# Kernel tuning notes

Hardware: AMD Instinct MI355X
Metric: run time of the kernel (lower is better)

## Reference

```python
import jax, jax.numpy as jnp
import numpy as np

INV_SQRT2 = 0.7071067811865476


def _dense(x, W):
    return jax.nn.silu(x @ W)


def _residual(x, Wa, Wb):
    # GemNet ResidualLayer: two activated dense layers, skip, 1/sqrt(2) rescale
    return (x + _dense(_dense(x, Wa), Wb)) * INV_SQRT2


def setup_inputs() -> dict:
    key = jax.random.key(0)
    ks = iter(jax.random.split(key, 40))
    N, E, T = 10000, 200000, 400000
    NR, NS = 128, 7          # num_radial, num_spherical
    A, M, Ti, To, C = 128, 256, 64, 64, 16
    NB = 2                   # num_blocks

    def w(shape):
        fan_in = shape[-2]
        return jax.random.normal(next(ks), shape, jnp.float32) / float(np.sqrt(fan_in))

    inp = {}
    inp['atomic_numbers'] = jax.random.randint(next(ks), (N,), 0, 120)
    inp['idx_s'] = jax.random.randint(next(ks), (E,), 0, N)
    inp['idx_t'] = jax.random.randint(next(ks), (E,), 0, N)
    inp['id3_ba'] = jax.random.randint(next(ks), (T,), 0, E)
    inp['id3_ca'] = jax.random.randint(next(ks), (T,), 0, E)
    inp['rbf'] = jax.random.uniform(next(ks), (E, NR), jnp.float32)
    inp['cbf'] = jax.random.normal(next(ks), (T, NS), jnp.float32)
    V = jax.random.normal(next(ks), (E, 3), jnp.float32)
    inp['V_st'] = V / jnp.linalg.norm(V, axis=-1, keepdims=True)
    inp['atom_table'] = jax.random.normal(next(ks), (120, A), jnp.float32)
    inp['W_edge_in'] = w((2 * A + NR, M))
    inp['rbf_w3'] = w((NB, NR, M))
    inp['W_down'] = w((NB, M, Ti))
    inp['W_cbf'] = w((NB, NS, C))
    inp['W_bil'] = jax.random.normal(next(ks), (NB, C, Ti, To), jnp.float32) / float(np.sqrt(C * Ti))
    inp['W_up'] = w((NB, To, M))
    inp['W_res_e'] = w((NB, 4, M, M))
    inp['rbf_wh'] = w((NB, NR, M))
    inp['W_e2a'] = w((NB, M, A))
    inp['W_res_a'] = w((NB, 2, A, A))
    inp['W_outE_in'] = w((A * (NB + 1), A))
    inp['W_outE_res'] = w((2, A, A))
    inp['W_outE_fin'] = w((A, 1))
    inp['W_outF_in'] = w((M * (NB + 1), M))
    inp['W_outF_res'] = w((2, M, M))
    inp['W_outF_fin'] = w((M, 1))
    return inp


def reference(atomic_numbers, idx_s, idx_t, id3_ba, id3_ca, rbf, cbf, V_st,
              atom_table, W_edge_in, rbf_w3, W_down, W_cbf, W_bil, W_up,
              W_res_e, rbf_wh, W_e2a, W_res_a,
              W_outE_in, W_outE_res, W_outE_fin,
              W_outF_in, W_outF_res, W_outF_fin):
    N = atomic_numbers.shape[0]
    E = idx_s.shape[0]
    NB = rbf_w3.shape[0]

    # atom and edge embeddings
    h = atom_table[atomic_numbers]                                       # [N, A]
    m = _dense(jnp.concatenate([h[idx_s], h[idx_t], rbf], axis=-1), W_edge_in)  # [E, M]

    xs_E = [h]
    xs_F = [m]
    for b in range(NB):
        # --- triplet interaction: edge -> triplet gather, bilinear CBF mix, scatter back ---
        x = (m * (rbf @ rbf_w3[b])) @ W_down[b]                          # [E, Ti]
        cb = cbf @ W_cbf[b]                                              # [T, C]
        y = jnp.einsum('tc,ti,cio->to', cb, x[id3_ba], W_bil[b])         # [T, To]
        agg = jax.ops.segment_sum(y, id3_ca, num_segments=E)             # [E, To]
        x3 = _dense(agg @ W_up[b], jnp.eye(x3_dim := W_up[b].shape[1], dtype=m.dtype)) if False else jax.nn.silu(agg @ W_up[b])  # [E, M]
        # --- residual / skip structure ---
        m2 = _residual(m, W_res_e[b, 0], W_res_e[b, 1])
        m2 = (m2 + x3) * INV_SQRT2
        m = _residual(m2, W_res_e[b, 2], W_res_e[b, 3])
        # --- atom update: edge -> atom scatter ---
        xa = (m * (rbf @ rbf_wh[b])) @ W_e2a[b]                          # [E, A]
        ha = jax.ops.segment_sum(xa, idx_t, num_segments=N)              # [N, A]
        h = h + _residual(ha, W_res_a[b, 0], W_res_a[b, 1])
        xs_E.append(h)
        xs_F.append(m)

    # FinalMLP-style heads over concatenated per-block features (emb*(num_blocks+1))
    xE = _residual(_dense(jnp.concatenate(xs_E, axis=-1), W_outE_in), W_outE_res[0], W_outE_res[1])
    E_atom = xE @ W_outE_fin                                             # [N, 1]
    xF = _residual(_dense(jnp.concatenate(xs_F, axis=-1), W_outF_in), W_outF_res[0], W_outF_res[1])
    F_edge = xF @ W_outF_fin                                             # [E, 1]
    forces = jax.ops.segment_sum(F_edge * V_st, idx_t, num_segments=N)   # [N, 3]
    return jnp.concatenate([E_atom, forces], axis=-1)                    # [N, 4]
```

## Files before the change

### kernel.cpp

```cpp
#include <hip/hip_runtime.h>
#include <hip/hip_bf16.h>
#include <cstdio>

#define INV2 0.70710678118654752440f
typedef __hip_bfloat16 bf16;
typedef __attribute__((ext_vector_type(8))) short short8v;
typedef __attribute__((ext_vector_type(8))) unsigned short u16x8;
typedef __attribute__((ext_vector_type(4))) float f32x4;

__device__ __forceinline__ float silu_f(float v) { return v / (1.0f + __expf(-v)); }
__device__ __forceinline__ float bf2f(unsigned short u) {
    union { unsigned int i; float f; } t; t.i = ((unsigned int)u) << 16; return t.f;
}
__device__ __forceinline__ unsigned short f2bf(float x) {
    bf16 b = __float2bfloat16(x);
    return *reinterpret_cast<unsigned short*>(&b);
}
__device__ __forceinline__ float toF(float v) { return v; }
__device__ __forceinline__ float toF(bf16 v) { return __bfloat162float(v); }
__device__ __forceinline__ void stF(float* p, float v) { *p = v; }
__device__ __forceinline__ void stF(bf16* p, float v) { *p = __float2bfloat16(v); }

__device__ __forceinline__ void ld8f(const float* p, float* o) {
    const float4 a = ((const float4*)p)[0], b = ((const float4*)p)[1];
    o[0]=a.x; o[1]=a.y; o[2]=a.z; o[3]=a.w; o[4]=b.x; o[5]=b.y; o[6]=b.z; o[7]=b.w;
}
__device__ __forceinline__ void ld8f(const bf16* p, float* o) {
    const u16x8 u = *(const u16x8*)p;
#pragma unroll
    for (int j = 0; j < 8; j++) o[j] = bf2f(u[j]);
}

__device__ __forceinline__ void gll16(const void* g, void* l) {
    __builtin_amdgcn_global_load_lds(
        (const __attribute__((address_space(1))) unsigned int*)g,
        (__attribute__((address_space(3))) unsigned int*)l, 16, 0, 0);
}

enum { AM_NORMAL = 0, AM_MUL2 = 1, AM_GATHER = 2, AM_SILU = 3, AM_DMA = 4 };
enum { EP_PLAIN = 0, EP_SILU = 1, EP_ACCUM = 2, EP_RES2 = 3, EP_RESADD = 4, EP_HEADRES = 5 };

__device__ __forceinline__ float epi_val(int EPI, float v, float c, float x) {
    if (EPI == EP_PLAIN)   return v;
    if (EPI == EP_SILU)    return silu_f(v);
    if (EPI == EP_ACCUM)   return c + v;
    if (EPI == EP_RES2)    return (c + silu_f(v)) * INV2;
    if (EPI == EP_RESADD)  return c + (x + silu_f(v)) * INV2;
           return (silu_f(x) + silu_f(v)) * INV2;
}

template <int AMODE, int EPI, int BN, typename AT, typename CT>
__global__ __launch_bounds__(256) void mgemm(
    const AT* __restrict__ A, const AT* __restrict__ A2,
    const int* __restrict__ gs, const int* __restrict__ gt,
    const bf16* __restrict__ Bt,
    CT* __restrict__ C, const CT* __restrict__ X,
    int Mrows, int Ncols, int K)
{
    constexpr bool DMA = (AMODE == AM_DMA);
    constexpr int AST = DMA ? 32 : 40;
    constexpr int FM = (BN == 128) ? 4 : 2;
    __shared__ __align__(16) unsigned short Als[128 * AST];
    __shared__ __align__(16) unsigned short Bls[BN * 32];
    const int tid = threadIdx.x;
    const int row0 = blockIdx.x * 128, col0 = blockIdx.y * BN;

    const int sr = tid >> 1;
    const int sh = (tid & 1) * 16;
    const int gr = row0 + sr;
    const bool rok = (gr < Mrows);
    int is_ = 0, it_ = 0;
    if (AMODE == AM_GATHER) { if (rok) { is_ = gs[gr]; it_ = gt[gr]; } }

    const int l = tid & 63, wid = tid >> 6;
    const int lr = l & 15;
    const int lk = (l >> 4) * 8;
    const int wrow = (BN == 128) ? ((wid & 1) * 64) : (wid * 32);
    const int wcol = (BN == 128) ? ((wid >> 1) * 64) : 0;

    f32x4 acc[FM][4];
#pragma unroll
    for (int i = 0; i < FM; i++)
#pragma unroll
        for (int j = 0; j < 4; j++)
#pragma unroll
            for (int q = 0; q < 4; q++) acc[i][j][q] = 0.f;

    for (int k0 = 0; k0 < K; k0 += 32) {
        if constexpr (DMA) {
#pragma unroll
            for (int i = 0; i < 2; i++) {
                const int c = i * 256 + tid;
                const int row = c >> 2;
                if (row0 + row < Mrows)
                    gll16(A + (size_t)(row0 + row) * K + k0 + (c & 3) * 8, &Als[c * 8]);
            }
        } else {
            float va[16];
            if (rok) {
                if (AMODE == AM_GATHER) {
                    const int reg = k0 >> 7, koff = (k0 & 127) + sh;
                    const AT* src = (reg == 0) ? (A + (size_t)is_ * 128 + koff)
                                  : (reg == 1) ? (A + (size_t)it_ * 128 + koff)
                                               : (A2 + (size_t)gr * 128 + koff);
                    ld8f(src, va); ld8f(src + 8, va + 8);
                } else {
                    const AT* src = A + (size_t)gr * K + k0 + sh;
                    ld8f(src, va); ld8f(src + 8, va + 8);
                    if (AMODE == AM_MUL2) {
                        float vb[16];
                        const AT* s2 = A2 + (size_t)gr * K + k0 + sh;
                        ld8f(s2, vb); ld8f(s2 + 8, vb + 8);
#pragma unroll
                        for (int j = 0; j < 16; j++) va[j] *= vb[j];
                    } else if (AMODE == AM_SILU) {
#pragma unroll
                        for (int j = 0; j < 16; j++) va[j] = silu_f(va[j]);
                    }
                }
            } else {
#pragma unroll
                for (int j = 0; j < 16; j++) va[j] = 0.f;
            }
            u16x8 av0, av1;
#pragma unroll
            for (int j = 0; j < 8; j++) { av0[j] = f2bf(va[j]); av1[j] = f2bf(va[j + 8]); }
            *(u16x8*)&Als[sr * AST + sh] = av0;
            *(u16x8*)&Als[sr * AST + sh + 8] = av1;
        }

#pragma unroll
        for (int i = 0; i < BN / 64; i++) {
            const int c = i * 256 + tid;
            gll16(Bt + (size_t)(col0 + (c >> 2)) * K + k0 + (c & 3) * 8, &Bls[c * 8]);
        }

        __syncthreads();

        short8v af[FM], bfr[4];
#pragma unroll
        for (int fm = 0; fm < FM; fm++)
            af[fm] = *(const short8v*)&Als[(wrow + fm * 16 + lr) * AST + lk];
#pragma unroll
        for (int fn = 0; fn < 4; fn++)
            bfr[fn] = *(const short8v*)&Bls[(wcol + fn * 16 + lr) * 32 + lk];
#pragma unroll
        for (int fm = 0; fm < FM; fm++)
#pragma unroll
            for (int fn = 0; fn < 4; fn++)
                acc[fm][fn] = __builtin_amdgcn_mfma_f32_16x16x32_bf16(
                    af[fm], bfr[fn], acc[fm][fn], 0, 0, 0);

        __syncthreads();
    }

#pragma unroll
    for (int fm = 0; fm < FM; fm++) {
        const int rb = row0 + wrow + fm * 16 + (l >> 4) * 4;
#pragma unroll
        for (int fn = 0; fn < 4; fn++) {
            const int c = col0 + wcol + fn * 16 + lr;
#pragma unroll
            for (int r = 0; r < 4; r++) {
                const int rr = rb + r;
                if (rr >= Mrows) continue;
                const size_t o = (size_t)rr * Ncols + c;
                stF(&C[o], epi_val(EPI, acc[fm][fn][r],
                                   (EPI >= EP_ACCUM) ? toF(C[o]) : 0.f,
                                   (EPI == EP_RESADD || EPI == EP_HEADRES) ? toF(X[o]) : 0.f));
            }
        }
    }
}

template <int AMODE, int EPI, typename AT, typename CT>
__global__ __launch_bounds__(512) void mgemm2(
    const AT* __restrict__ A, const AT* __restrict__ A2,
    const int* __restrict__ gs, const int* __restrict__ gt,
    const bf16* __restrict__ Bt,
    CT* __restrict__ C, const CT* __restrict__ X,
    int Mrows, int K)
{
    constexpr bool DMA = (AMODE == AM_DMA);
    constexpr int AST = DMA ? 32 : 40;
    __shared__ __align__(16) unsigned short Als[128 * AST];
    __shared__ __align__(16) unsigned short Bls[256 * 32];
    const int tid = threadIdx.x;
    const int row0 = blockIdx.x * 128;

    const int sr = tid >> 2;
    const int sh = (tid & 3) * 8;
    const int gr = row0 + sr;
    const bool rok = (gr < Mrows);
    int is_ = 0, it_ = 0;
    if (AMODE == AM_GATHER) { if (rok) { is_ = gs[gr]; it_ = gt[gr]; } }

    const int l = tid & 63, wid = tid >> 6;
    const int lr = l & 15;
    const int lk = (l >> 4) * 8;
    const int wrow = (wid & 1) * 64;
    const int wcol = (wid >> 1) * 64;

    f32x4 acc[4][4];
#pragma unroll
    for (int i = 0; i < 4; i++)
#pragma unroll
        for (int j = 0; j < 4; j++)
#pragma unroll
            for (int q = 0; q < 4; q++) acc[i][j][q] = 0.f;

    for (int k0 = 0; k0 < K; k0 += 32) {
        if constexpr (DMA) {
            const int c = tid, row = c >> 2;
            if (row0 + row < Mrows)
                gll16(A + (size_t)(row0 + row) * K + k0 + (c & 3) * 8, &Als[c * 8]);
        } else {
            float va[8];
            if (rok) {
                if (AMODE == AM_GATHER) {
                    const int reg = k0 >> 7, koff = (k0 & 127) + sh;
                    const AT* src = (reg == 0) ? (A + (size_t)is_ * 128 + koff)
                                  : (reg == 1) ? (A + (size_t)it_ * 128 + koff)
                                               : (A2 + (size_t)gr * 128 + koff);
                    ld8f(src, va);
                } else {
                    ld8f(A + (size_t)gr * K + k0 + sh, va);
                    if (AMODE == AM_MUL2) {
                        float vb[8];
                        ld8f(A2 + (size_t)gr * K + k0 + sh, vb);
#pragma unroll
                        for (int j = 0; j < 8; j++) va[j] *= vb[j];
                    } else if (AMODE == AM_SILU) {
#pragma unroll
                        for (int j = 0; j < 8; j++) va[j] = silu_f(va[j]);
                    }
                }
            } else {
#pragma unroll
                for (int j = 0; j < 8; j++) va[j] = 0.f;
            }
            u16x8 av;
#pragma unroll
            for (int j = 0; j < 8; j++) av[j] = f2bf(va[j]);
            *(u16x8*)&Als[sr * AST + sh] = av;
        }

#pragma unroll
        for (int i = 0; i < 2; i++) {
            const int c = i * 512 + tid;
            gll16(Bt + (size_t)(c >> 2) * K + k0 + (c & 3) * 8, &Bls[c * 8]);
        }

        __syncthreads();

        short8v af[4], bfr[4];
#pragma unroll
        for (int fm = 0; fm < 4; fm++)
            af[fm] = *(const short8v*)&Als[(wrow + fm * 16 + lr) * AST + lk];
#pragma unroll
        for (int fn = 0; fn < 4; fn++)
            bfr[fn] = *(const short8v*)&Bls[(wcol + fn * 16 + lr) * 32 + lk];
#pragma unroll
        for (int fm = 0; fm < 4; fm++)
#pragma unroll
            for (int fn = 0; fn < 4; fn++)
                acc[fm][fn] = __builtin_amdgcn_mfma_f32_16x16x32_bf16(
                    af[fm], bfr[fn], acc[fm][fn], 0, 0, 0);

        __syncthreads();
    }

#pragma unroll
    for (int fm = 0; fm < 4; fm++) {
        const int rb = row0 + wrow + fm * 16 + (l >> 4) * 4;
#pragma unroll
        for (int fn = 0; fn < 4; fn++) {
            const int c = wcol + fn * 16 + lr;
#pragma unroll
            for (int r = 0; r < 4; r++) {
                const int rr = rb + r;
                if (rr >= Mrows) continue;
                const size_t o = (size_t)rr * 256 + c;
                stF(&C[o], epi_val(EPI, acc[fm][fn][r],
                                   (EPI >= EP_ACCUM) ? toF(C[o]) : 0.f,
                                   (EPI == EP_RESADD || EPI == EP_HEADRES) ? toF(X[o]) : 0.f));
            }
        }
    }
}

__global__ __launch_bounds__(256) void trip_gemm(
    const bf16* __restrict__ x,
    const bf16* __restrict__ cb,
    const int* __restrict__ ba, const int* __restrict__ ca,
    const bf16* __restrict__ BtT,
    float* __restrict__ agg)
{
    __shared__ __align__(16) unsigned short At[128 * 40];
    __shared__ __align__(16) unsigned short Bs[64 * 40];
    const int tid = threadIdx.x;
    const int gr0 = blockIdx.x * 128;

    const int sr = tid >> 1, sh = tid & 1;
    const int gr = gr0 + sr;
    const int e = ba[gr];
    float xr[32];
    {
        const bf16* xp = x + (size_t)e * 64 + sh * 16;
        const u16x8 a0 = *(const u16x8*)xp;
        const u16x8 a1 = *(const u16x8*)(xp + 8);
        const u16x8 b0 = *(const u16x8*)(xp + 32);
        const u16x8 b1 = *(const u16x8*)(xp + 40);
#pragma unroll
        for (int j = 0; j < 8; j++) {
            xr[j] = bf2f(a0[j]); xr[8 + j] = bf2f(a1[j]);
            xr[16 + j] = bf2f(b0[j]); xr[24 + j] = bf2f(b1[j]);
        }
    }
    float cbr[16];
    {
        const u16x8 c0 = *(const u16x8*)(cb + (size_t)gr * 16);
        const u16x8 c1 = *(const u16x8*)(cb + (size_t)gr * 16 + 8);
#pragma unroll
        for (int j = 0; j < 8; j++) { cbr[j] = bf2f(c0[j]); cbr[8 + j] = bf2f(c1[j]); }
    }

    const int l = tid & 63, wv = tid >> 6;
    const int lr = l & 15, lg = l >> 4, lk = lg * 8;
    const int wrow = wv * 32;
    const int bcol = tid >> 2, bq = tid & 3;

    f32x4 acc[2][4];
#pragma unroll
    for (int i = 0; i < 2; i++)
#pragma unroll
        for (int j = 0; j < 4; j++)
#pragma unroll
            for (int q = 0; q < 4; q++) acc[i][j][q] = 0.f;

#pragma unroll 4
    for (int ks = 0; ks < 32; ++ks) {
        const float cbv = cbr[ks >> 1];
        const int ib = (ks & 1) * 16;
        u16x8 p0, p1;
#pragma unroll
        for (int j = 0; j < 8; j++) {
            p0[j] = f2bf(cbv * xr[ib + j]);
            p1[j] = f2bf(cbv * xr[ib + 8 + j]);
        }
        *(u16x8*)&At[sr * 40 + sh * 16] = p0;
        *(u16x8*)&At[sr * 40 + sh * 16 + 8] = p1;
        const u16x8 bv8 = *(const u16x8*)(BtT + (size_t)bcol * 1024 + ks * 32 + bq * 8);
        *(u16x8*)&Bs[bcol * 40 + bq * 8] = bv8;
        __syncthreads();

        short8v af[2], bf4[4];
        af[0] = *(const short8v*)&At[(wrow + lr) * 40 + lk];
        af[1] = *(const short8v*)&At[(wrow + 16 + lr) * 40 + lk];
#pragma unroll
        for (int fn = 0; fn < 4; fn++)
            bf4[fn] = *(const short8v*)&Bs[(fn * 16 + lr) * 40 + lk];
#pragma unroll
        for (int fm = 0; fm < 2; fm++)
#pragma unroll
            for (int fn = 0; fn < 4; fn++)
                acc[fm][fn] = __builtin_amdgcn_mfma_f32_16x16x32_bf16(
                    af[fm], bf4[fn], acc[fm][fn], 0, 0, 0);
        __syncthreads();
    }

#pragma unroll
    for (int fm = 0; fm < 2; fm++)
#pragma unroll
        for (int q = 0; q < 4; q++) {
            const int rr = wrow + fm * 16 + lg * 4 + q;
            const int eo = ca[gr0 + rr];
#pragma unroll
            for (int fn = 0; fn < 4; fn++)
                atomicAdd(&agg[(size_t)eo * 64 + fn * 16 + lr], acc[fm][fn][q]);
        }
}

__global__ __launch_bounds__(256) void cb16(const float* __restrict__ cbf,
                                            const float* __restrict__ Wcb,
                                            bf16* __restrict__ cb, int T)
{
    const int gid = blockIdx.x * 256 + threadIdx.x;
    const int t = gid >> 4, c = gid & 15;
    if (t >= T) return;
    const float* cr = cbf + (size_t)t * 7;
    float s = 0.f;
#pragma unroll
    for (int k = 0; k < 7; k++) s += cr[k] * Wcb[k * 16 + c];
    cb[(size_t)t * 16 + c] = __float2bfloat16(s);
}

struct TJob { const float* src; bf16* dst; int K; int N; };
struct TJobs { TJob j[40]; };

__global__ __launch_bounds__(256) void transpose_weights(TJobs JB) {
    const TJob J = JB.j[blockIdx.y];
    const int total = J.K * J.N;
    const int gid = blockIdx.x * 256 + threadIdx.x;
    if (gid >= total) return;
    const int n = gid / J.K, k = gid - n * J.K;
    J.dst[(size_t)n * J.K + k] = __float2bfloat16(J.src[(size_t)k * J.N + n]);
}

__global__ __launch_bounds__(256) void embed_h(const int* __restrict__ z,
                                               const float* __restrict__ tab,
                                               float* __restrict__ h, int N)
{
    const int gid = blockIdx.x * 256 + threadIdx.x;
    const int n = gid >> 7, j = gid & 127;
    if (n >= N) return;
    h[(size_t)n * 128 + j] = tab[(size_t)z[n] * 128 + j];
}

__global__ __launch_bounds__(256) void scatter_ha(const bf16* __restrict__ xa,
                                                  const int* __restrict__ idxt,
                                                  float* __restrict__ ha, int E)
{
    const int gid = blockIdx.x * 256 + threadIdx.x;
    const int e = gid >> 7, j = gid & 127;
    if (e >= E) return;
    atomicAdd(&ha[(size_t)idxt[e] * 128 + j], toF(xa[(size_t)e * 128 + j]));
}

template <typename AT>
__global__ __launch_bounds__(256) void rowdot(const AT* __restrict__ Xm,
                                              const float* __restrict__ w,
                                              float* __restrict__ outv,
                                              int rows, int width, int ostride)
{
    const int wid = (blockIdx.x * 256 + threadIdx.x) >> 6;
    const int lane = threadIdx.x & 63;
    if (wid >= rows) return;
    float s = 0.f;
    for (int q = lane; q < width; q += 64) s += toF(Xm[(size_t)wid * width + q]) * w[q];
#pragma unroll
    for (int off = 32; off > 0; off >>= 1) s += __shfl_down(s, off);
    if (lane == 0) outv[(size_t)wid * ostride] = s;
}

__global__ __launch_bounds__(256) void scatter_forces(const float* __restrict__ Fe,
                                                      const float* __restrict__ Vst,
                                                      const int* __restrict__ idxt,
                                                      float* __restrict__ out, int E)
{
    const int e = blockIdx.x * 256 + threadIdx.x;
    if (e >= E) return;
    const float f = Fe[e];
    const int n = idxt[e];
    atomicAdd(&out[(size_t)n * 4 + 1], f * Vst[(size_t)e * 3 + 0]);
    atomicAdd(&out[(size_t)n * 4 + 2], f * Vst[(size_t)e * 3 + 1]);
    atomicAdd(&out[(size_t)n * 4 + 3], f * Vst[(size_t)e * 3 + 2]);
}

#define MG(AM, EP, BNv, Aptr, A2p, GS, GT, Btp, Cp, Xp, MR, NC, KK)                       \
    mgemm<AM, EP, BNv><<<dim3(((MR) + 127) / 128, (NC) / (BNv)), 256, 0, stream>>>(       \
        Aptr, A2p, GS, GT, Btp, Cp, Xp, MR, NC, KK)

#define MG2(AM, EP, Aptr, A2p, GS, GT, Btp, Cp, Xp, MR, KK)                               \
    mgemm2<AM, EP><<<((MR) + 127) / 128, 512, 0, stream>>>(                               \
        Aptr, A2p, GS, GT, Btp, Cp, Xp, MR, KK)

extern "C" void kernel_launch(void* const* d_in, const int* in_sizes, int n_in,
                              void* d_out, int out_size, void* d_ws, size_t ws_size,
                              hipStream_t stream)
{
    const int N = in_sizes[0];
    const int E = in_sizes[1];
    const int T = in_sizes[3];
    const int NB = 2;

    const int*   z        = (const int*)d_in[0];
    const int*   idx_s    = (const int*)d_in[1];
    const int*   idx_t    = (const int*)d_in[2];
    const int*   id3_ba   = (const int*)d_in[3];
    const int*   id3_ca   = (const int*)d_in[4];
    const float* rbf      = (const float*)d_in[5];
    const float* cbf      = (const float*)d_in[6];
    const float* V_st     = (const float*)d_in[7];
    const float* atom_tab = (const float*)d_in[8];
    const float* W_edge_in= (const float*)d_in[9];
    const float* rbf_w3   = (const float*)d_in[10];
    const float* W_down   = (const float*)d_in[11];
    const float* W_cbf    = (const float*)d_in[12];
    const float* W_bil    = (const float*)d_in[13];
    const float* W_up     = (const float*)d_in[14];
    const float* W_res_e  = (const float*)d_in[15];
    const float* rbf_wh   = (const float*)d_in[16];
    const float* W_e2a    = (const float*)d_in[17];
    const float* W_res_a  = (const float*)d_in[18];
    const float* W_outE_in  = (const float*)d_in[19];
    const float* W_outE_res = (const float*)d_in[20];
    const float* W_outE_fin = (const float*)d_in[21];
    const float* W_outF_in  = (const float*)d_in[22];
    const float* W_outF_res = (const float*)d_in[23];
    const float* W_outF_fin = (const float*)d_in[24];

    float* out = (float*)d_out;

    char* base = (char*)d_ws;
    size_t off = 0;
    auto alloc = [&](size_t nbytes) { char* p = base + off; off += (nbytes + 15) & ~(size_t)15; return p; };
    bf16*  m_cur = (bf16*)alloc((size_t)E * 256 * 2);
    bf16*  headF = (bf16*)alloc((size_t)E * 256 * 2);
    bf16*  S1    = (bf16*)alloc((size_t)E * 256 * 2);
    float* agg   = (float*)alloc((size_t)E * 64 * 4);
    bf16*  xbuf  = (bf16*)alloc((size_t)E * 64 * 2);
    float* h_cur = (float*)alloc((size_t)N * 128 * 4);
    float* headE = (float*)alloc((size_t)N * 128 * 4);
    float* ha    = (float*)alloc((size_t)N * 128 * 4);
    float* tA    = (float*)alloc((size_t)N * 128 * 4);
    bf16 *bt_outF[3], *bt_outE[3], *bt_r3[2], *bt_down[2], *bt_bilT[2], *bt_up[2],
         *bt_rese[8], *bt_rh[2], *bt_e2a[2], *bt_resa[4], *bt_Fres[2], *bt_Eres[2];
    bf16* bt_edge = (bf16*)alloc(384 * 256 * 2);
    for (int s = 0; s < 3; s++) bt_outF[s] = (bf16*)alloc(256 * 256 * 2);
    for (int s = 0; s < 3; s++) bt_outE[s] = (bf16*)alloc(128 * 128 * 2);
    for (int b = 0; b < 2; b++) bt_r3[b]   = (bf16*)alloc(256 * 128 * 2);
    for (int b = 0; b < 2; b++) bt_down[b] = (bf16*)alloc(64 * 256 * 2);
    for (int b = 0; b < 2; b++) bt_bilT[b] = (bf16*)alloc(64 * 1024 * 2);
    for (int b = 0; b < 2; b++) bt_up[b]   = (bf16*)alloc(256 * 64 * 2);
    for (int i = 0; i < 8; i++) bt_rese[i] = (bf16*)alloc(256 * 256 * 2);
    for (int b = 0; b < 2; b++) bt_rh[b]   = (bf16*)alloc(256 * 128 * 2);
    for (int b = 0; b < 2; b++) bt_e2a[b]  = (bf16*)alloc(128 * 256 * 2);
    for (int i = 0; i < 4; i++) bt_resa[i] = (bf16*)alloc(128 * 128 * 2);
    for (int i = 0; i < 2; i++) bt_Fres[i] = (bf16*)alloc(256 * 256 * 2);
    for (int i = 0; i < 2; i++) bt_Eres[i] = (bf16*)alloc(128 * 128 * 2);
    if (off > ws_size) {
        fprintf(stderr, "kernel_launch: ws too small: need %zu have %zu\n", off, ws_size);
        return;
    }
    bf16*  xa = (bf16*)agg;
    float* Fe = (float*)xbuf;
    float* xE = ha;
    bf16*  cbS = S1;

    const float* nfp = nullptr;
    const bf16*  nbp = nullptr;
    const int*   nip = nullptr;

    {
        TJobs JB; int nj = 0;
        auto addj = [&](const float* s, bf16* d, int K, int Nn) { JB.j[nj++] = TJob{s, d, K, Nn}; };
        addj(W_edge_in, bt_edge, 384, 256);
        for (int s = 0; s < 3; s++) addj(W_outF_in + (size_t)s * 256 * 256, bt_outF[s], 256, 256);
        for (int s = 0; s < 3; s++) addj(W_outE_in + (size_t)s * 128 * 128, bt_outE[s], 128, 128);
        for (int b = 0; b < 2; b++) addj(rbf_w3 + (size_t)b * 128 * 256, bt_r3[b], 128, 256);
        for (int b = 0; b < 2; b++) addj(W_down + (size_t)b * 256 * 64, bt_down[b], 256, 64);
        for (int b = 0; b < 2; b++) addj(W_bil + (size_t)b * 65536, bt_bilT[b], 1024, 64);
        for (int b = 0; b < 2; b++) addj(W_up + (size_t)b * 64 * 256, bt_up[b], 64, 256);
        for (int i = 0; i < 8; i++) addj(W_res_e + (size_t)i * 65536, bt_rese[i], 256, 256);
        for (int b = 0; b < 2; b++) addj(rbf_wh + (size_t)b * 128 * 256, bt_rh[b], 128, 256);
        for (int b = 0; b < 2; b++) addj(W_e2a + (size_t)b * 256 * 128, bt_e2a[b], 256, 128);
        for (int i = 0; i < 4; i++) addj(W_res_a + (size_t)i * 16384, bt_resa[i], 128, 128);
        for (int i = 0; i < 2; i++) addj(W_outF_res + (size_t)i * 65536, bt_Fres[i], 256, 256);
        for (int i = 0; i < 2; i++) addj(W_outE_res + (size_t)i * 16384, bt_Eres[i], 128, 128);
        transpose_weights<<<dim3(384, nj), 256, 0, stream>>>(JB);
    }

    embed_h<<<(N * 128 + 255) / 256, 256, 0, stream>>>(z, atom_tab, h_cur, N);
    MG2(AM_GATHER, EP_SILU, h_cur, rbf, idx_s, idx_t, bt_edge, m_cur, nbp, E, 384);
    MG2(AM_DMA, EP_PLAIN, m_cur, nbp, nip, nip, bt_outF[0], headF, nbp, E, 256);
    MG(AM_NORMAL, EP_PLAIN, 64, h_cur, nfp, nip, nip, bt_outE[0], headE, nfp, N, 128, 128);

    for (int b = 0; b < NB; ++b) {
        const float* Wcb = W_cbf + (size_t)b * 7 * 16;

        MG2(AM_NORMAL, EP_PLAIN, rbf, nfp, nip, nip, bt_r3[b], S1, nbp, E, 128);
        MG(AM_MUL2, EP_PLAIN, 64, m_cur, S1, nip, nip, bt_down[b], xbuf, nbp, E, 64, 256);
        cb16<<<(T * 16 + 255) / 256, 256, 0, stream>>>(cbf, Wcb, cbS, T);
        (void)hipMemsetAsync(agg, 0, (size_t)E * 64 * sizeof(float), stream);
        trip_gemm<<<T / 128, 256, 0, stream>>>(xbuf, cbS, id3_ba, id3_ca, bt_bilT[b], agg);

        MG2(AM_DMA, EP_SILU, m_cur, nbp, nip, nip, bt_rese[4 * b + 0], S1, nbp, E, 256);
        MG2(AM_DMA, EP_RES2, S1, nbp, nip, nip, bt_rese[4 * b + 1], m_cur, nbp, E, 256);
        MG2(AM_NORMAL, EP_RES2, agg, nfp, nip, nip, bt_up[b], m_cur, nbp, E, 64);
        MG2(AM_DMA, EP_SILU, m_cur, nbp, nip, nip, bt_rese[4 * b + 2], S1, nbp, E, 256);
        MG2(AM_DMA, EP_RES2, S1, nbp, nip, nip, bt_rese[4 * b + 3], m_cur, nbp, E, 256);
        MG2(AM_DMA, EP_ACCUM, m_cur, nbp, nip, nip, bt_outF[b + 1], headF, nbp, E, 256);

        MG2(AM_NORMAL, EP_PLAIN, rbf, nfp, nip, nip, bt_rh[b], S1, nbp, E, 128);
        MG(AM_MUL2, EP_PLAIN, 128, m_cur, S1, nip, nip, bt_e2a[b], xa, nbp, E, 128, 256);
        (void)hipMemsetAsync(ha, 0, (size_t)N * 128 * sizeof(float), stream);
        scatter_ha<<<(E * 128 + 255) / 256, 256, 0, stream>>>(xa, idx_t, ha, E);
        MG(AM_NORMAL, EP_SILU, 64, ha, nfp, nip, nip, bt_resa[2 * b + 0], tA, nfp, N, 128, 128);
        MG(AM_NORMAL, EP_RESADD, 64, tA, nfp, nip, nip, bt_resa[2 * b + 1], h_cur, ha, N, 128, 128);
        MG(AM_NORMAL, EP_ACCUM, 64, h_cur, nfp, nip, nip, bt_outE[b + 1], headE, nfp, N, 128, 128);
    }

    MG2(AM_SILU, EP_SILU, headF, nbp, nip, nip, bt_Fres[0], S1, nbp, E, 256);
    MG2(AM_DMA, EP_HEADRES, S1, nbp, nip, nip, bt_Fres[1], m_cur, headF, E, 256);
    rowdot<<<(E * 64 + 255) / 256, 256, 0, stream>>>(m_cur, W_outF_fin, Fe, E, 256, 1);

    (void)hipMemsetAsync(out, 0, (size_t)out_size * sizeof(float), stream);
    MG(AM_SILU, EP_SILU, 64, headE, nfp, nip, nip, bt_Eres[0], tA, nfp, N, 128, 128);
    MG(AM_NORMAL, EP_HEADRES, 64, tA, nfp, nip, nip, bt_Eres[1], xE, headE, N, 128, 128);
    rowdot<<<(N * 64 + 255) / 256, 256, 0, stream>>>(xE, W_outE_fin, out, N, 128, 4);
    scatter_forces<<<(E + 255) / 256, 256, 0, stream>>>(Fe, V_st, idx_t, out, E);
}
```

Measured before the change: 2.695 ms.

## Fuse shared-input edge GEMMs and residual-plus-up projection into dual-output kernels

Adds mgemm2d, which computes two GEMMs that share the same A operand (the first residual dense layer and the head-F projection) in one pass. It also adds mgemm2x, which fuses the second residual layer and the up-projection of agg with their combined residual epilogue. The head-F accumulation for each block's m is moved earlier so it can share the load of m_cur, and the last block's contribution now runs after the loop. This removes repeated reads of the E x 256 activations and several kernel launches, at the cost of larger shared memory, more accumulator registers and a 512-thread block size.

```diff
diff --git a/kernel.cpp b/kernel.cpp
--- a/kernel.cpp
+++ b/kernel.cpp
@@ -284,6 +284,189 @@
                 stF(&C[o], epi_val(EPI, acc[fm][fn][r],
                                    (EPI >= EP_ACCUM) ? toF(C[o]) : 0.f,
                                    (EPI == EP_RESADD || EPI == EP_HEADRES) ? toF(X[o]) : 0.f));
+            }
+        }
+    }
+}
+
+template <int EPI2>
+__global__ __launch_bounds__(512) void mgemm2d(
+    const bf16* __restrict__ A,
+    const bf16* __restrict__ Bt1, const bf16* __restrict__ Bt2,
+    bf16* __restrict__ C1, bf16* __restrict__ C2, int Mrows)
+{
+    __shared__ __align__(16) unsigned short Als[128 * 32];
+    __shared__ __align__(16) unsigned short B1ls[256 * 32];
+    __shared__ __align__(16) unsigned short B2ls[256 * 32];
+    const int tid = threadIdx.x;
+    const int row0 = blockIdx.x * 128;
+
+    const int l = tid & 63, wid = tid >> 6;
+    const int lr = l & 15;
+    const int lk = (l >> 4) * 8;
+    const int wrow = (wid & 1) * 64;
+    const int wcol = (wid >> 1) * 64;
+
+    f32x4 acc1[4][4], acc2[4][4];
+#pragma unroll
+    for (int i = 0; i < 4; i++)
+#pragma unroll
+        for (int j = 0; j < 4; j++)
+#pragma unroll
+            for (int q = 0; q < 4; q++) { acc1[i][j][q] = 0.f; acc2[i][j][q] = 0.f; }
+
+    for (int k0 = 0; k0 < 256; k0 += 32) {
+        {
+            const int row = tid >> 2;
+            if (row0 + row < Mrows)
+                gll16(A + (size_t)(row0 + row) * 256 + k0 + (tid & 3) * 8, &Als[tid * 8]);
+        }
+#pragma unroll
+        for (int i = 0; i < 2; i++) {
+            const int c = i * 512 + tid;
+            gll16(Bt1 + (size_t)(c >> 2) * 256 + k0 + (c & 3) * 8, &B1ls[c * 8]);
+            gll16(Bt2 + (size_t)(c >> 2) * 256 + k0 + (c & 3) * 8, &B2ls[c * 8]);
+        }
+        __syncthreads();
+
+        short8v af[4], b1[4], b2[4];
+#pragma unroll
+        for (int fm = 0; fm < 4; fm++)
+            af[fm] = *(const short8v*)&Als[(wrow + fm * 16 + lr) * 32 + lk];
+#pragma unroll
+        for (int fn = 0; fn < 4; fn++) {
+            b1[fn] = *(const short8v*)&B1ls[(wcol + fn * 16 + lr) * 32 + lk];
+            b2[fn] = *(const short8v*)&B2ls[(wcol + fn * 16 + lr) * 32 + lk];
+        }
+#pragma unroll
+        for (int fm = 0; fm < 4; fm++)
+#pragma unroll
+            for (int fn = 0; fn < 4; fn++) {
+                acc1[fm][fn] = __builtin_amdgcn_mfma_f32_16x16x32_bf16(af[fm], b1[fn], acc1[fm][fn], 0, 0, 0);
+                acc2[fm][fn] = __builtin_amdgcn_mfma_f32_16x16x32_bf16(af[fm], b2[fn], acc2[fm][fn], 0, 0, 0);
+            }
+        __syncthreads();
+    }
+
+#pragma unroll
+    for (int fm = 0; fm < 4; fm++) {
+        const int rb = row0 + wrow + fm * 16 + (l >> 4) * 4;
+#pragma unroll
+        for (int fn = 0; fn < 4; fn++) {
+            const int c = wcol + fn * 16 + lr;
+#pragma unroll
+            for (int r = 0; r < 4; r++) {
+                const int rr = rb + r;
+                if (rr >= Mrows) continue;
+                const size_t o = (size_t)rr * 256 + c;
+                stF(&C1[o], silu_f(acc1[fm][fn][r]));
+                stF(&C2[o], (EPI2 == EP_ACCUM) ? toF(C2[o]) + acc2[fm][fn][r]
+                                               : acc2[fm][fn][r]);
+            }
+        }
+    }
+}
+
+__global__ __launch_bounds__(512) void mgemm2x(
+    const bf16* __restrict__ S1, const bf16* __restrict__ BtWe1,
+    const float* __restrict__ agg, const bf16* __restrict__ BtUp,
+    bf16* __restrict__ M, int Mrows)
+{
+    __shared__ __align__(16) unsigned short Als[128 * 32];
+    __shared__ __align__(16) unsigned short Bls[256 * 32];
+    const int tid = threadIdx.x;
+    const int row0 = blockIdx.x * 128;
+
+    const int l = tid & 63, wid = tid >> 6;
+    const int lr = l & 15;
+    const int lk = (l >> 4) * 8;
+    const int wrow = (wid & 1) * 64;
+    const int wcol = (wid >> 1) * 64;
+
+    f32x4 acc1[4][4], acc2[4][4];
+#pragma unroll
+    for (int i = 0; i < 4; i++)
+#pragma unroll
+        for (int j = 0; j < 4; j++)
+#pragma unroll
+            for (int q = 0; q < 4; q++) { acc1[i][j][q] = 0.f; acc2[i][j][q] = 0.f; }
+
+    for (int k0 = 0; k0 < 256; k0 += 32) {
+        {
+            const int row = tid >> 2;
+            if (row0 + row < Mrows)
+                gll16(S1 + (size_t)(row0 + row) * 256 + k0 + (tid & 3) * 8, &Als[tid * 8]);
+        }
+#pragma unroll
+        for (int i = 0; i < 2; i++) {
+            const int c = i * 512 + tid;
+            gll16(BtWe1 + (size_t)(c >> 2) * 256 + k0 + (c & 3) * 8, &Bls[c * 8]);
+        }
+        __syncthreads();
+        short8v af[4], bfr[4];
+#pragma unroll
+        for (int fm = 0; fm < 4; fm++)
+            af[fm] = *(const short8v*)&Als[(wrow + fm * 16 + lr) * 32 + lk];
+#pragma unroll
+        for (int fn = 0; fn < 4; fn++)
+            bfr[fn] = *(const short8v*)&Bls[(wcol + fn * 16 + lr) * 32 + lk];
+#pragma unroll
+        for (int fm = 0; fm < 4; fm++)
+#pragma unroll
+            for (int fn = 0; fn < 4; fn++)
+                acc1[fm][fn] = __builtin_amdgcn_mfma_f32_16x16x32_bf16(af[fm], bfr[fn], acc1[fm][fn], 0, 0, 0);
+        __syncthreads();
+    }
+
+    const int sr = tid >> 2;
+    const int sh = (tid & 3) * 8;
+    for (int k0 = 0; k0 < 64; k0 += 32) {
+        {
+            float va[8];
+            if (row0 + sr < Mrows) ld8f(agg + (size_t)(row0 + sr) * 64 + k0 + sh, va);
+            else {
+#pragma unroll
+                for (int j = 0; j < 8; j++) va[j] = 0.f;
+            }
+            u16x8 av;
+#pragma unroll
+            for (int j = 0; j < 8; j++) av[j] = f2bf(va[j]);
+            *(u16x8*)&Als[sr * 32 + sh] = av;
+        }
+#pragma unroll
+        for (int i = 0; i < 2; i++) {
+            const int c = i * 512 + tid;
+            gll16(BtUp + (size_t)(c >> 2) * 64 + k0 + (c & 3) * 8, &Bls[c * 8]);
+        }
+        __syncthreads();
+        short8v af[4], bfr[4];
+#pragma unroll
+        for (int fm = 0; fm < 4; fm++)
+            af[fm] = *(const short8v*)&Als[(wrow + fm * 16 + lr) * 32 + lk];
+#pragma unroll
+        for (int fn = 0; fn < 4; fn++)
+            bfr[fn] = *(const short8v*)&Bls[(wcol + fn * 16 + lr) * 32 + lk];
+#pragma unroll
+        for (int fm = 0; fm < 4; fm++)
+#pragma unroll
+            for (int fn = 0; fn < 4; fn++)
+                acc2[fm][fn] = __builtin_amdgcn_mfma_f32_16x16x32_bf16(af[fm], bfr[fn], acc2[fm][fn], 0, 0, 0);
+        __syncthreads();
+    }
+
+#pragma unroll
+    for (int fm = 0; fm < 4; fm++) {
+        const int rb = row0 + wrow + fm * 16 + (l >> 4) * 4;
+#pragma unroll
+        for (int fn = 0; fn < 4; fn++) {
+            const int c = wcol + fn * 16 + lr;
+#pragma unroll
+            for (int r = 0; r < 4; r++) {
+                const int rr = rb + r;
+                if (rr >= Mrows) continue;
+                const size_t o = (size_t)rr * 256 + c;
+                const float m2 = (toF(M[o]) + silu_f(acc1[fm][fn][r])) * INV2;
+                stF(&M[o], (m2 + silu_f(acc2[fm][fn][r])) * INV2);
             }
         }
     }
@@ -563,9 +746,9 @@
 
     embed_h<<<(N * 128 + 255) / 256, 256, 0, stream>>>(z, atom_tab, h_cur, N);
     MG2(AM_GATHER, EP_SILU, h_cur, rbf, idx_s, idx_t, bt_edge, m_cur, nbp, E, 384);
-    MG2(AM_DMA, EP_PLAIN, m_cur, nbp, nip, nip, bt_outF[0], headF, nbp, E, 256);
     MG(AM_NORMAL, EP_PLAIN, 64, h_cur, nfp, nip, nip, bt_outE[0], headE, nfp, N, 128, 128);
 
+    const int gE = (E + 127) / 128;
     for (int b = 0; b < NB; ++b) {
         const float* Wcb = W_cbf + (size_t)b * 7 * 16;
 
@@ -575,12 +758,15 @@
         (void)hipMemsetAsync(agg, 0, (size_t)E * 64 * sizeof(float), stream);
         trip_gemm<<<T / 128, 256, 0, stream>>>(xbuf, cbS, id3_ba, id3_ca, bt_bilT[b], agg);
 
-        MG2(AM_DMA, EP_SILU, m_cur, nbp, nip, nip, bt_rese[4 * b + 0], S1, nbp, E, 256);
-        MG2(AM_DMA, EP_RES2, S1, nbp, nip, nip, bt_rese[4 * b + 1], m_cur, nbp, E, 256);
-        MG2(AM_NORMAL, EP_RES2, agg, nfp, nip, nip, bt_up[b], m_cur, nbp, E, 64);
+        if (b == 0)
+            mgemm2d<EP_PLAIN><<<gE, 512, 0, stream>>>(m_cur, bt_rese[0], bt_outF[0], S1, headF, E);
+        else
+            mgemm2d<EP_ACCUM><<<gE, 512, 0, stream>>>(m_cur, bt_rese[4], bt_outF[1], S1, headF, E);
+
+        mgemm2x<<<gE, 512, 0, stream>>>(S1, bt_rese[4 * b + 1], agg, bt_up[b], m_cur, E);
+
         MG2(AM_DMA, EP_SILU, m_cur, nbp, nip, nip, bt_rese[4 * b + 2], S1, nbp, E, 256);
         MG2(AM_DMA, EP_RES2, S1, nbp, nip, nip, bt_rese[4 * b + 3], m_cur, nbp, E, 256);
-        MG2(AM_DMA, EP_ACCUM, m_cur, nbp, nip, nip, bt_outF[b + 1], headF, nbp, E, 256);
 
         MG2(AM_NORMAL, EP_PLAIN, rbf, nfp, nip, nip, bt_rh[b], S1, nbp, E, 128);
         MG(AM_MUL2, EP_PLAIN, 128, m_cur, S1, nip, nip, bt_e2a[b], xa, nbp, E, 128, 256);
@@ -591,6 +777,8 @@
         MG(AM_NORMAL, EP_ACCUM, 64, h_cur, nfp, nip, nip, bt_outE[b + 1], headE, nfp, N, 128, 128);
     }
 
+    MG2(AM_DMA, EP_ACCUM, m_cur, nbp, nip, nip, bt_outF[2], headF, nbp, E, 256);
+
     MG2(AM_SILU, EP_SILU, headF, nbp, nip, nip, bt_Fres[0], S1, nbp, E, 256);
     MG2(AM_DMA, EP_HEADRES, S1, nbp, nip, nip, bt_Fres[1], m_cur, headF, E, 256);
     rowdot<<<(E * 64 + 255) / 256, 256, 0, stream>>>(m_cur, W_outF_fin, Fe, E, 256, 1);
```

After: 2.709 ms. No clear change (+0.5%).
